# Performance work log

Hardware: AMD Instinct MI355X
Metric: run time of the kernel (lower is better)

Reference implementation:

```python
import jax, jax.numpy as jnp
import numpy as np

BN_EPS = 1e-5
NUM_HEADS = 4
PROJ = 512

def _bn(x, gamma, beta, mean, var):
    # eval-mode BatchNorm1d over last dim
    return (x - mean) * jax.lax.rsqrt(var + BN_EPS) * gamma + beta

def setup_inputs() -> dict:
    key = jax.random.key(0)
    ks = jax.random.split(key, 12)
    B, Tq, Tk, D = 32, 256, 1024, 512
    inp = {
        "s": jax.random.normal(ks[0], (B, Tq, D), jnp.float32),
        "h": jax.random.normal(ks[1], (B, Tk, D), jnp.float32),
        "phi_gamma": jnp.ones((D,), jnp.float32),
        "phi_beta": jnp.zeros((D,), jnp.float32),
        "phi_mean": 0.1 * jax.random.normal(ks[2], (D,), jnp.float32),
        "phi_var": jax.random.uniform(ks[3], (D,), jnp.float32, 0.5, 1.5),
        "W_phi": 0.02 * jax.random.normal(ks[4], (PROJ * NUM_HEADS, D), jnp.float32),
        "psi_gamma": jnp.ones((D,), jnp.float32),
        "psi_beta": jnp.zeros((D,), jnp.float32),
        "psi_mean": 0.1 * jax.random.normal(ks[5], (D,), jnp.float32),
        "psi_var": jax.random.uniform(ks[6], (D,), jnp.float32, 0.5, 1.5),
        "W_psi": 0.02 * jax.random.normal(ks[7], (PROJ, D), jnp.float32),
        "red_gamma": jnp.ones((D * NUM_HEADS,), jnp.float32),
        "red_beta": jnp.zeros((D * NUM_HEADS,), jnp.float32),
        "red_mean": 0.1 * jax.random.normal(ks[8], (D * NUM_HEADS,), jnp.float32),
        "red_var": jax.random.uniform(ks[9], (D * NUM_HEADS,), jnp.float32, 0.5, 1.5),
        "W_red": 0.02 * jax.random.normal(ks[10], (D, D * NUM_HEADS), jnp.float32),
    }
    return inp

def reference(s, h, phi_gamma, phi_beta, phi_mean, phi_var, W_phi,
              psi_gamma, psi_beta, psi_mean, psi_var, W_psi,
              red_gamma, red_beta, red_mean, red_var, W_red):
    B, Tq, _ = s.shape
    # phi: BN + Linear on decoder states -> (B, Tq, H*PROJ)
    ms = _bn(s, phi_gamma, phi_beta, phi_mean, phi_var) @ W_phi.T
    # psi: BN + Linear on encoder states -> (B, Tk, PROJ)
    mh = _bn(h, psi_gamma, psi_beta, psi_mean, psi_var) @ W_psi.T
    # split heads along last dim of ms (matches torch.split order)
    ms4 = ms.reshape(B, Tq, NUM_HEADS, PROJ)
    # unscaled dot-product scores per head: (H, B, Tq, Tk)
    e = jnp.einsum("bqhd,bkd->hbqk", ms4, mh)
    a = jax.nn.softmax(e, axis=-1)
    # context uses the ORIGINAL h (not mh): (B, Tq, H, D) -> concat heads
    ctx = jnp.einsum("hbqk,bkv->bqhv", a, h).reshape(B, Tq, -1)
    # reduce: BN + Linear -> (B, Tq, D)
    c = _bn(ctx, red_gamma, red_beta, red_mean, red_var) @ W_red.T
    return (a, c)
```

## Files before the change

kernel.cpp:

```cpp
#include <hip/hip_runtime.h>

typedef short s8v __attribute__((ext_vector_type(8)));
typedef float f4v __attribute__((ext_vector_type(4)));

static constexpr int Bc = 32, Tq = 256, Tkc = 1024, Dc = 512, Hc = 4;
static constexpr float BN_EPS = 1e-5f;

__device__ inline ushort f2bf(float x) {
    union { float f; unsigned int u; } v; v.f = x;
    unsigned int r = v.u + 0x7fff + ((v.u >> 16) & 1);
    return (ushort)(r >> 16);
}

__global__ __launch_bounds__(256) void fold_bn(
    const float* __restrict__ W, const float* __restrict__ gamma,
    const float* __restrict__ beta, const float* __restrict__ mean,
    const float* __restrict__ var, ushort* __restrict__ Wp,
    float* __restrict__ bias, int K)
{
    int n = blockIdx.x;
    int tid = threadIdx.x;
    float acc = 0.f;
    for (int k = tid; k < K; k += 256) {
        float sc = gamma[k] * rsqrtf(var[k] + BN_EPS);
        float sh = beta[k] - mean[k] * sc;
        float w = W[(long)n * K + k];
        Wp[(long)n * K + k] = f2bf(w * sc);
        acc = fmaf(w, sh, acc);
    }
    __shared__ float red[256];
    red[tid] = acc;
    __syncthreads();
    for (int s = 128; s > 0; s >>= 1) {
        if (tid < s) red[tid] += red[tid + s];
        __syncthreads();
    }
    if (tid == 0) bias[n] = red[0];
}

__global__ __launch_bounds__(256) void f32_to_bf16(
    const float* __restrict__ x, ushort* __restrict__ y)
{
    long i = ((long)blockIdx.x * 256 + threadIdx.x) * 4;
    float4 v = *(const float4*)&x[i];
    ushort4 o = { f2bf(v.x), f2bf(v.y), f2bf(v.z), f2bf(v.w) };
    *(ushort4*)&y[i] = o;
}

__global__ __launch_bounds__(256) void transpose_bf16(
    const float* __restrict__ h, ushort* __restrict__ hT)
{
    __shared__ float tl[64][65];
    int b = blockIdx.z, k0 = blockIdx.y * 64, d0 = blockIdx.x * 64;
    int t = threadIdx.x, r = t >> 4, c = (t & 15) * 4;
    const float* hb = h + ((long)b * Tkc + k0) * Dc + d0;
    #pragma unroll
    for (int i = 0; i < 4; i++) {
        float4 v = *(const float4*)&hb[(long)(r + i * 16) * Dc + c];
        tl[r + i * 16][c + 0] = v.x; tl[r + i * 16][c + 1] = v.y;
        tl[r + i * 16][c + 2] = v.z; tl[r + i * 16][c + 3] = v.w;
    }
    __syncthreads();
    ushort* o = hT + ((long)b * Dc + d0) * Tkc + k0;
    #pragma unroll
    for (int i = 0; i < 4; i++) {
        int dr = r + i * 16;
        ushort4 ov = { f2bf(tl[c + 0][dr]), f2bf(tl[c + 1][dr]),
                       f2bf(tl[c + 2][dr]), f2bf(tl[c + 3][dr]) };
        *(ushort4*)&o[(long)dr * Tkc + c] = ov;
    }
}

typedef __attribute__((address_space(1))) void gvoid;
typedef __attribute__((address_space(3))) void lvoid;

__global__ __launch_bounds__(256) void gemm_mfma(
    const ushort* __restrict__ A, const ushort* __restrict__ B,
    float* __restrict__ Cf, ushort* __restrict__ Cb,
    const float* __restrict__ bias,
    int K, int lda, int ldb, int ldc,
    long sAh, long sAb, long sBb, long sCh, long sCb, int nB)
{
    int z = blockIdx.z;
    int hh = z / nB, bb = z - hh * nB;
    A += hh * sAh + bb * sAb;
    B += bb * sBb;
    long coff = hh * sCh + bb * sCb;

    __shared__ ushort Als[128 * 32];
    __shared__ ushort Bls[128 * 32];

    int tid = threadIdx.x;
    int l = tid & 63, w = tid >> 6;
    int m0 = blockIdx.y * 128, n0 = blockIdx.x * 128;

    int L0 = (w * 2 + 0) * 64 + l;
    int L1 = (w * 2 + 1) * 64 + l;
    int am0 = L0 >> 2, ac0 = (L0 & 3) ^ ((am0 >> 1) & 3);
    int am1 = L1 >> 2, ac1 = (L1 & 3) ^ ((am1 >> 1) & 3);
    const ushort* gA0 = A + (long)(m0 + am0) * lda + ac0 * 8;
    const ushort* gA1 = A + (long)(m0 + am1) * lda + ac1 * 8;
    const ushort* gB0 = B + (long)(n0 + am0) * ldb + ac0 * 8;
    const ushort* gB1 = B + (long)(n0 + am1) * ldb + ac1 * 8;
    ushort* lA0 = &Als[(w * 2 + 0) * 512];
    ushort* lA1 = &Als[(w * 2 + 1) * 512];
    ushort* lB0 = &Bls[(w * 2 + 0) * 512];
    ushort* lB1 = &Bls[(w * 2 + 1) * 512];

    int wm = (w >> 1) * 64, wn = (w & 1) * 64;
    int fr = l & 15, kc = l >> 4;

    int aidx[4], bidx[4];
    #pragma unroll
    for (int t = 0; t < 4; t++) {
        int ra = wm + t * 16 + fr;
        aidx[t] = (ra * 4 + (kc ^ ((ra >> 1) & 3))) * 8;
        int rb = wn + t * 16 + fr;
        bidx[t] = (rb * 4 + (kc ^ ((rb >> 1) & 3))) * 8;
    }

    f4v acc[4][4] = {};

    for (int k0 = 0; k0 < K; k0 += 32) {
        __builtin_amdgcn_global_load_lds((gvoid*)(gA0 + k0), (lvoid*)lA0, 16, 0, 0);
        __builtin_amdgcn_global_load_lds((gvoid*)(gA1 + k0), (lvoid*)lA1, 16, 0, 0);
        __builtin_amdgcn_global_load_lds((gvoid*)(gB0 + k0), (lvoid*)lB0, 16, 0, 0);
        __builtin_amdgcn_global_load_lds((gvoid*)(gB1 + k0), (lvoid*)lB1, 16, 0, 0);
        __syncthreads();

        s8v af[4], bfv[4];
        #pragma unroll
        for (int t = 0; t < 4; t++) af[t]  = *(const s8v*)&Als[aidx[t]];
        #pragma unroll
        for (int t = 0; t < 4; t++) bfv[t] = *(const s8v*)&Bls[bidx[t]];
        #pragma unroll
        for (int i = 0; i < 4; i++)
            #pragma unroll
            for (int j = 0; j < 4; j++)
                acc[i][j] = __builtin_amdgcn_mfma_f32_16x16x32_bf16(
                    af[i], bfv[j], acc[i][j], 0, 0, 0);
        __syncthreads();
    }

    #pragma unroll
    for (int i = 0; i < 4; i++) {
        #pragma unroll
        for (int j = 0; j < 4; j++) {
            int n = n0 + wn + j * 16 + fr;
            float bv = bias ? bias[n] : 0.f;
            #pragma unroll
            for (int r = 0; r < 4; r++) {
                int m = m0 + wm + i * 16 + kc * 4 + r;
                float v = acc[i][j][r] + bv;
                long off = coff + (long)m * ldc + n;
                if (Cb) Cb[off] = f2bf(v);
                else    Cf[off] = v;
            }
        }
    }
}

__global__ __launch_bounds__(256) void softmax_rows(
    float* __restrict__ E, ushort* __restrict__ Abf)
{
    int wave = threadIdx.x >> 6;
    int lane = threadIdx.x & 63;
    long row = (long)blockIdx.x * 4 + wave;
    float4* rp = (float4*)(E + row * 1024);
    ushort* op = Abf + row * 1024;

    float4 v[4];
    float mx = -3.4e38f;
    #pragma unroll
    for (int i = 0; i < 4; i++) {
        v[i] = rp[lane + (i << 6)];
        mx = fmaxf(mx, fmaxf(fmaxf(v[i].x, v[i].y), fmaxf(v[i].z, v[i].w)));
    }
    #pragma unroll
    for (int o = 32; o > 0; o >>= 1) mx = fmaxf(mx, __shfl_xor(mx, o, 64));

    float sum = 0.f;
    #pragma unroll
    for (int i = 0; i < 4; i++) {
        v[i].x = __expf(v[i].x - mx);
        v[i].y = __expf(v[i].y - mx);
        v[i].z = __expf(v[i].z - mx);
        v[i].w = __expf(v[i].w - mx);
        sum += v[i].x + v[i].y + v[i].z + v[i].w;
    }
    #pragma unroll
    for (int o = 32; o > 0; o >>= 1) sum += __shfl_xor(sum, o, 64);

    float inv = 1.f / sum;
    #pragma unroll
    for (int i = 0; i < 4; i++) {
        v[i].x *= inv; v[i].y *= inv; v[i].z *= inv; v[i].w *= inv;
        rp[lane + (i << 6)] = v[i];
        ushort4 ov = { f2bf(v[i].x), f2bf(v[i].y), f2bf(v[i].z), f2bf(v[i].w) };
        *(ushort4*)&op[(lane + (i << 6)) * 4] = ov;
    }
}

extern "C" void kernel_launch(void* const* d_in, const int* in_sizes, int n_in,
                              void* d_out, int out_size, void* d_ws, size_t ws_size,
                              hipStream_t stream)
{
    const float* s     = (const float*)d_in[0];
    const float* h     = (const float*)d_in[1];
    const float* phi_g = (const float*)d_in[2];
    const float* phi_b = (const float*)d_in[3];
    const float* phi_m = (const float*)d_in[4];
    const float* phi_v = (const float*)d_in[5];
    const float* W_phi = (const float*)d_in[6];
    const float* psi_g = (const float*)d_in[7];
    const float* psi_b = (const float*)d_in[8];
    const float* psi_m = (const float*)d_in[9];
    const float* psi_v = (const float*)d_in[10];
    const float* W_psi = (const float*)d_in[11];
    const float* red_g = (const float*)d_in[12];
    const float* red_b = (const float*)d_in[13];
    const float* red_m = (const float*)d_in[14];
    const float* red_v = (const float*)d_in[15];
    const float* W_red = (const float*)d_in[16];

    float* out_a = (float*)d_out;
    float* out_c = out_a + (long)Hc * Bc * Tq * Tkc;

    char* p = (char*)d_ws;
    ushort* Wphi_b = (ushort*)p;  p += (long)2048 * 512 * 2;
    ushort* Wpsi_b = (ushort*)p;  p += (long)512 * 512 * 2;
    ushort* Wred_b = (ushort*)p;  p += (long)512 * 2048 * 2;
    float* bias_phi = (float*)p;  p += 2048 * 4;
    float* bias_psi = (float*)p;  p += 512 * 4;
    float* bias_red = (float*)p;  p += 512 * 4;
    ushort* s_bf  = (ushort*)p;   p += (long)8192 * 512 * 2;
    ushort* h_bf  = (ushort*)p;   p += (long)32768 * 512 * 2;
    ushort* hT_bf = (ushort*)p;   p += (long)32768 * 512 * 2;
    ushort* ms_bf = (ushort*)p;   p += (long)8192 * 2048 * 2;
    ushort* mh_bf = (ushort*)p;   p += (long)32768 * 512 * 2;
    ushort* a_bf  = ms_bf;
    ushort* ctx_bf = s_bf;

    fold_bn<<<2048, 256, 0, stream>>>(W_phi, phi_g, phi_b, phi_m, phi_v, Wphi_b, bias_phi, 512);
    fold_bn<<<512,  256, 0, stream>>>(W_psi, psi_g, psi_b, psi_m, psi_v, Wpsi_b, bias_psi, 512);
    fold_bn<<<512,  256, 0, stream>>>(W_red, red_g, red_b, red_m, red_v, Wred_b, bias_red, 2048);

    f32_to_bf16<<<4096,  256, 0, stream>>>(s, s_bf);
    f32_to_bf16<<<16384, 256, 0, stream>>>(h, h_bf);
    transpose_bf16<<<dim3(8, 16, 32), 256, 0, stream>>>(h, hT_bf);

    gemm_mfma<<<dim3(16, 64, 1), 256, 0, stream>>>(
        s_bf, Wphi_b, nullptr, ms_bf, bias_phi,
        512, 512, 512, 2048, 0, 0, 0, 0, 0, 1);

    gemm_mfma<<<dim3(4, 256, 1), 256, 0, stream>>>(
        h_bf, Wpsi_b, nullptr, mh_bf, bias_psi,
        512, 512, 512, 512, 0, 0, 0, 0, 0, 1);

    gemm_mfma<<<dim3(8, 2, Hc * Bc), 256, 0, stream>>>(
        ms_bf, mh_bf, out_a, nullptr, nullptr,
        512, 2048, 512, 1024,
         512,  (long)Tq * 2048,
         (long)Tkc * 512,
         (long)Bc * Tq * Tkc,  (long)Tq * Tkc, Bc);

    softmax_rows<<<(Hc * Bc * Tq) / 4, 256, 0, stream>>>(out_a, a_bf);

    gemm_mfma<<<dim3(4, 2, Hc * Bc), 256, 0, stream>>>(
        a_bf, hT_bf, nullptr, ctx_bf, nullptr,
        1024, 1024, 1024, 2048,
         (long)Bc * Tq * Tkc,  (long)Tq * Tkc,
         (long)Dc * Tkc,
         512,  (long)Tq * 2048, Bc);

    gemm_mfma<<<dim3(4, 64, 1), 256, 0, stream>>>(
        ctx_bf, Wred_b, out_c, nullptr, bias_red,
        2048, 2048, 2048, 512, 0, 0, 0, 0, 0, 1);
}
```

Before: 619.5 us.

## Deepen GEMM K-tile, flatten grid, fuse h conversion, split-K final GEMM

Result: faster. 535.9 us (-13.5%).

```diff
diff --git a/kernel.cpp b/kernel.cpp
--- a/kernel.cpp
+++ b/kernel.cpp
@@ -47,18 +47,23 @@
     *(ushort4*)&y[i] = o;
 }
 
-__global__ __launch_bounds__(256) void transpose_bf16(
-    const float* __restrict__ h, ushort* __restrict__ hT)
+__global__ __launch_bounds__(256) void conv_h(
+    const float* __restrict__ h, ushort* __restrict__ h_bf,
+    ushort* __restrict__ hT)
 {
     __shared__ float tl[64][65];
     int b = blockIdx.z, k0 = blockIdx.y * 64, d0 = blockIdx.x * 64;
     int t = threadIdx.x, r = t >> 4, c = (t & 15) * 4;
     const float* hb = h + ((long)b * Tkc + k0) * Dc + d0;
-    #pragma unroll
-    for (int i = 0; i < 4; i++) {
-        float4 v = *(const float4*)&hb[(long)(r + i * 16) * Dc + c];
-        tl[r + i * 16][c + 0] = v.x; tl[r + i * 16][c + 1] = v.y;
-        tl[r + i * 16][c + 2] = v.z; tl[r + i * 16][c + 3] = v.w;
+    ushort* sb = h_bf + ((long)b * Tkc + k0) * Dc + d0;
+    #pragma unroll
+    for (int i = 0; i < 4; i++) {
+        int rr = r + i * 16;
+        float4 v = *(const float4*)&hb[(long)rr * Dc + c];
+        tl[rr][c + 0] = v.x; tl[rr][c + 1] = v.y;
+        tl[rr][c + 2] = v.z; tl[rr][c + 3] = v.w;
+        ushort4 sv = { f2bf(v.x), f2bf(v.y), f2bf(v.z), f2bf(v.w) };
+        *(ushort4*)&sb[(long)rr * Dc + c] = sv;
     }
     __syncthreads();
     ushort* o = hT + ((long)b * Dc + d0) * Tkc + k0;
@@ -71,90 +76,111 @@
     }
 }
 
+__global__ __launch_bounds__(256) void init_c(
+    float* __restrict__ C, const float* __restrict__ bias)
+{
+    long i = (long)blockIdx.x * 256 + threadIdx.x;
+    int n4 = (int)(i & 127);
+    float4 b = ((const float4*)bias)[n4];
+    ((float4*)C)[i] = b;
+}
+
 typedef __attribute__((address_space(1))) void gvoid;
 typedef __attribute__((address_space(3))) void lvoid;
 
-__global__ __launch_bounds__(256) void gemm_mfma(
+__global__ __launch_bounds__(256, 4) void gemm_mfma(
     const ushort* __restrict__ A, const ushort* __restrict__ B,
     float* __restrict__ Cf, ushort* __restrict__ Cb,
-    const float* __restrict__ bias,
+    const float* __restrict__ bias, int atom,
     int K, int lda, int ldb, int ldc,
-    long sAh, long sAb, long sBb, long sCh, long sCb, int nB)
-{
-    int z = blockIdx.z;
+    long sAh, long sAb, long sBh, long sBb, long sCh, long sCb,
+    int nB, int nxs, int zbits)
+{
+    int bx = blockIdx.x;
+    int z = bx & ((1 << zbits) - 1);
+    int j2 = bx >> zbits;
+    int gx = j2 & ((1 << nxs) - 1);
+    int gy = j2 >> nxs;
+
     int hh = z / nB, bb = z - hh * nB;
     A += hh * sAh + bb * sAb;
-    B += bb * sBb;
+    B += hh * sBh + bb * sBb;
     long coff = hh * sCh + bb * sCb;
 
-    __shared__ ushort Als[128 * 32];
-    __shared__ ushort Bls[128 * 32];
+    __shared__ ushort Als[128 * 64];
+    __shared__ ushort Bls[128 * 64];
 
     int tid = threadIdx.x;
     int l = tid & 63, w = tid >> 6;
-    int m0 = blockIdx.y * 128, n0 = blockIdx.x * 128;
-
-    int L0 = (w * 2 + 0) * 64 + l;
-    int L1 = (w * 2 + 1) * 64 + l;
-    int am0 = L0 >> 2, ac0 = (L0 & 3) ^ ((am0 >> 1) & 3);
-    int am1 = L1 >> 2, ac1 = (L1 & 3) ^ ((am1 >> 1) & 3);
-    const ushort* gA0 = A + (long)(m0 + am0) * lda + ac0 * 8;
-    const ushort* gA1 = A + (long)(m0 + am1) * lda + ac1 * 8;
-    const ushort* gB0 = B + (long)(n0 + am0) * ldb + ac0 * 8;
-    const ushort* gB1 = B + (long)(n0 + am1) * ldb + ac1 * 8;
-    ushort* lA0 = &Als[(w * 2 + 0) * 512];
-    ushort* lA1 = &Als[(w * 2 + 1) * 512];
-    ushort* lB0 = &Bls[(w * 2 + 0) * 512];
-    ushort* lB1 = &Bls[(w * 2 + 1) * 512];
+    int m0 = gy * 128, n0 = gx * 128;
+
+    const ushort* gA[4]; const ushort* gB[4];
+    ushort* lA[4]; ushort* lB[4];
+    #pragma unroll
+    for (int j = 0; j < 4; j++) {
+        int L = (w * 4 + j) * 64 + l;
+        int m = L >> 3, c = L & 7;
+        int kof = (c ^ ((m >> 1) & 7)) * 8;
+        gA[j] = A + (long)(m0 + m) * lda + kof;
+        gB[j] = B + (long)(n0 + m) * ldb + kof;
+        lA[j] = &Als[(w * 4 + j) * 512];
+        lB[j] = &Bls[(w * 4 + j) * 512];
+    }
 
     int wm = (w >> 1) * 64, wn = (w & 1) * 64;
     int fr = l & 15, kc = l >> 4;
 
-    int aidx[4], bidx[4];
-    #pragma unroll
-    for (int t = 0; t < 4; t++) {
-        int ra = wm + t * 16 + fr;
-        aidx[t] = (ra * 4 + (kc ^ ((ra >> 1) & 3))) * 8;
-        int rb = wn + t * 16 + fr;
-        bidx[t] = (rb * 4 + (kc ^ ((rb >> 1) & 3))) * 8;
-    }
+    int aidx[2][4], bidx[2][4];
+    #pragma unroll
+    for (int kk = 0; kk < 2; kk++)
+        #pragma unroll
+        for (int t = 0; t < 4; t++) {
+            int ra = wm + t * 16 + fr;
+            aidx[kk][t] = (ra * 8 + ((kk * 4 + kc) ^ ((ra >> 1) & 7))) * 8;
+            int rb = wn + t * 16 + fr;
+            bidx[kk][t] = (rb * 8 + ((kk * 4 + kc) ^ ((rb >> 1) & 7))) * 8;
+        }
 
     f4v acc[4][4] = {};
 
-    for (int k0 = 0; k0 < K; k0 += 32) {
-        __builtin_amdgcn_global_load_lds((gvoid*)(gA0 + k0), (lvoid*)lA0, 16, 0, 0);
-        __builtin_amdgcn_global_load_lds((gvoid*)(gA1 + k0), (lvoid*)lA1, 16, 0, 0);
-        __builtin_amdgcn_global_load_lds((gvoid*)(gB0 + k0), (lvoid*)lB0, 16, 0, 0);
-        __builtin_amdgcn_global_load_lds((gvoid*)(gB1 + k0), (lvoid*)lB1, 16, 0, 0);
-        __syncthreads();
-
-        s8v af[4], bfv[4];
-        #pragma unroll
-        for (int t = 0; t < 4; t++) af[t]  = *(const s8v*)&Als[aidx[t]];
-        #pragma unroll
-        for (int t = 0; t < 4; t++) bfv[t] = *(const s8v*)&Bls[bidx[t]];
-        #pragma unroll
-        for (int i = 0; i < 4; i++)
-            #pragma unroll
-            for (int j = 0; j < 4; j++)
-                acc[i][j] = __builtin_amdgcn_mfma_f32_16x16x32_bf16(
-                    af[i], bfv[j], acc[i][j], 0, 0, 0);
-        __syncthreads();
-    }
-
-    #pragma unroll
-    for (int i = 0; i < 4; i++) {
+    for (int k0 = 0; k0 < K; k0 += 64) {
         #pragma unroll
         for (int j = 0; j < 4; j++) {
-            int n = n0 + wn + j * 16 + fr;
+            __builtin_amdgcn_global_load_lds((gvoid*)(gA[j] + k0), (lvoid*)lA[j], 16, 0, 0);
+            __builtin_amdgcn_global_load_lds((gvoid*)(gB[j] + k0), (lvoid*)lB[j], 16, 0, 0);
+        }
+        __syncthreads();
+        #pragma unroll
+        for (int kk = 0; kk < 2; kk++) {
+            s8v af[4], bfv[4];
+            #pragma unroll
+            for (int t = 0; t < 4; t++) af[t]  = *(const s8v*)&Als[aidx[kk][t]];
+            #pragma unroll
+            for (int t = 0; t < 4; t++) bfv[t] = *(const s8v*)&Bls[bidx[kk][t]];
+            #pragma unroll
+            for (int i = 0; i < 4; i++)
+                #pragma unroll
+                for (int jj = 0; jj < 4; jj++)
+                    acc[i][jj] = __builtin_amdgcn_mfma_f32_16x16x32_bf16(
+                        af[i], bfv[jj], acc[i][jj], 0, 0, 0);
+        }
+        __syncthreads();
+    }
+
+    #pragma unroll
+    for (int i = 0; i < 4; i++) {
+        #pragma unroll
+        for (int jj = 0; jj < 4; jj++) {
+            int n = n0 + wn + jj * 16 + fr;
             float bv = bias ? bias[n] : 0.f;
             #pragma unroll
             for (int r = 0; r < 4; r++) {
                 int m = m0 + wm + i * 16 + kc * 4 + r;
-                float v = acc[i][j][r] + bv;
+                float v = acc[i][jj][r] + bv;
                 long off = coff + (long)m * ldc + n;
-                if (Cb) Cb[off] = f2bf(v);
-                else    Cf[off] = v;
+                if (atom)    atomicAdd(&Cf[off], v);
+                else if (Cb) Cb[off] = f2bf(v);
+                else         Cf[off] = v;
             }
         }
     }
@@ -245,35 +271,41 @@
     fold_bn<<<512,  256, 0, stream>>>(W_psi, psi_g, psi_b, psi_m, psi_v, Wpsi_b, bias_psi, 512);
     fold_bn<<<512,  256, 0, stream>>>(W_red, red_g, red_b, red_m, red_v, Wred_b, bias_red, 2048);
 
-    f32_to_bf16<<<4096,  256, 0, stream>>>(s, s_bf);
-    f32_to_bf16<<<16384, 256, 0, stream>>>(h, h_bf);
-    transpose_bf16<<<dim3(8, 16, 32), 256, 0, stream>>>(h, hT_bf);
-
-    gemm_mfma<<<dim3(16, 64, 1), 256, 0, stream>>>(
-        s_bf, Wphi_b, nullptr, ms_bf, bias_phi,
-        512, 512, 512, 2048, 0, 0, 0, 0, 0, 1);
-
-    gemm_mfma<<<dim3(4, 256, 1), 256, 0, stream>>>(
-        h_bf, Wpsi_b, nullptr, mh_bf, bias_psi,
-        512, 512, 512, 512, 0, 0, 0, 0, 0, 1);
-
-    gemm_mfma<<<dim3(8, 2, Hc * Bc), 256, 0, stream>>>(
-        ms_bf, mh_bf, out_a, nullptr, nullptr,
+    f32_to_bf16<<<4096, 256, 0, stream>>>(s, s_bf);
+    conv_h<<<dim3(8, 16, 32), 256, 0, stream>>>(h, h_bf, hT_bf);
+    init_c<<<4096, 256, 0, stream>>>(out_c, bias_red);
+
+    gemm_mfma<<<16 * 64, 256, 0, stream>>>(
+        s_bf, Wphi_b, nullptr, ms_bf, bias_phi, 0,
+        512, 512, 512, 2048, 0, 0, 0, 0, 0, 0, 1, 4, 0);
+
+    gemm_mfma<<<4 * 256, 256, 0, stream>>>(
+        h_bf, Wpsi_b, nullptr, mh_bf, bias_psi, 0,
+        512, 512, 512, 512, 0, 0, 0, 0, 0, 0, 1, 2, 0);
+
+    gemm_mfma<<<8 * 2 * 128, 256, 0, stream>>>(
+        ms_bf, mh_bf, out_a, nullptr, nullptr, 0,
         512, 2048, 512, 1024,
          512,  (long)Tq * 2048,
-         (long)Tkc * 512,
-         (long)Bc * Tq * Tkc,  (long)Tq * Tkc, Bc);
+         0,  (long)Tkc * 512,
+         (long)Bc * Tq * Tkc,  (long)Tq * Tkc,
+        Bc, 3, 7);
 
     softmax_rows<<<(Hc * Bc * Tq) / 4, 256, 0, stream>>>(out_a, a_bf);
 
-    gemm_mfma<<<dim3(4, 2, Hc * Bc), 256, 0, stream>>>(
-        a_bf, hT_bf, nullptr, ctx_bf, nullptr,
+    gemm_mfma<<<4 * 2 * 128, 256, 0, stream>>>(
+        a_bf, hT_bf, nullptr, ctx_bf, nullptr, 0,
         1024, 1024, 1024, 2048,
          (long)Bc * Tq * Tkc,  (long)Tq * Tkc,
-         (long)Dc * Tkc,
-         512,  (long)Tq * 2048, Bc);
-
-    gemm_mfma<<<dim3(4, 64, 1), 256, 0, stream>>>(
-        ctx_bf, Wred_b, out_c, nullptr, bias_red,
-        2048, 2048, 2048, 512, 0, 0, 0, 0, 0, 1);
-}
+         0,  (long)Dc * Tkc,
+         512,  (long)Tq * 2048,
+        Bc, 2, 7);
+
+    gemm_mfma<<<4 * 64 * 4, 256, 0, stream>>>(
+        ctx_bf, Wred_b, out_c, nullptr, nullptr, 1,
+        512, 2048, 2048, 512,
+         512,  0,
+         512,  0,
+         0,  0,
+        1, 2, 2);
+}
```
